# Performance work log

Measured on AMD Instinct MI355X. Metric: run time of the kernel, lower is better.

## Reference

```python
import jax, jax.numpy as jnp
import numpy as np

E = 256      # feat_dim
H = 4        # num_heads
D = E // H   # head_dim = 64
NC = 7       # num_classes
B = 65536
EPS = 1e-5


def layernorm(x, g, b):
    mu = jnp.mean(x, axis=-1, keepdims=True)
    var = jnp.mean((x - mu) ** 2, axis=-1, keepdims=True)
    return (x - mu) * jax.lax.rsqrt(var + EPS) * g + b


def setup_inputs() -> dict:
    key = jax.random.key(0)
    ks = jax.random.split(key, 16)
    s = 0.02
    return {
        "f_swin":   jax.random.normal(ks[0], (B, E), jnp.float32),
        "f_maxvit": jax.random.normal(ks[1], (B, E), jnp.float32),
        "f_focal":  jax.random.normal(ks[2], (B, E), jnp.float32),
        # MultiheadAttention params (torch packs q,k,v into in_proj)
        "in_proj_w": jax.random.normal(ks[3], (3 * E, E), jnp.float32) * s,
        "in_proj_b": jnp.zeros((3 * E,), jnp.float32),
        "out_w": jax.random.normal(ks[4], (E, E), jnp.float32) * s,
        "out_b": jnp.zeros((E,), jnp.float32),
        # fusion LayerNorm
        "ln1_g": jnp.ones((E,), jnp.float32),
        "ln1_b": jnp.zeros((E,), jnp.float32),
        # gate: Linear(3E, 3)
        "gate_w": jax.random.normal(ks[5], (3, 3 * E), jnp.float32) * s,
        "gate_b": jnp.zeros((3,), jnp.float32),
        # deep_head: LN -> Linear(E,256) -> GELU -> Linear(256,128) -> GELU -> Linear(128,7)
        "ln2_g": jnp.ones((E,), jnp.float32),
        "ln2_b": jnp.zeros((E,), jnp.float32),
        "w1": jax.random.normal(ks[6], (256, E), jnp.float32) * s,
        "b1": jnp.zeros((256,), jnp.float32),
        "w2": jax.random.normal(ks[7], (128, 256), jnp.float32) * s,
        "b2": jnp.zeros((128,), jnp.float32),
        "w3": jax.random.normal(ks[8], (NC, 128), jnp.float32) * s,
        "b3": jnp.zeros((NC,), jnp.float32),
    }


def reference(f_swin, f_maxvit, f_focal, in_proj_w, in_proj_b, out_w, out_b,
              ln1_g, ln1_b, gate_w, gate_b, ln2_g, ln2_b,
              w1, b1, w2, b2, w3, b3):
    # --- AttentionFusionModule ---
    stacked = jnp.stack([f_swin, f_maxvit, f_focal], axis=1)  # [B,3,E]
    qkv = stacked @ in_proj_w.T + in_proj_b                   # [B,3,3E]
    q, k, v = jnp.split(qkv, 3, axis=-1)
    # [B,3,E] -> [B,H,3,D]
    def to_heads(t):
        return t.reshape(t.shape[0], 3, H, D).transpose(0, 2, 1, 3)
    qh, kh, vh = to_heads(q), to_heads(k), to_heads(v)
    scores = jnp.einsum('bhqd,bhkd->bhqk', qh, kh) / jnp.sqrt(jnp.float32(D))
    attn = jax.nn.softmax(scores, axis=-1)
    ctx = jnp.einsum('bhqk,bhkd->bhqd', attn, vh)             # [B,H,3,D]
    ctx = ctx.transpose(0, 2, 1, 3).reshape(-1, 3, E)         # [B,3,E]
    att_out = ctx @ out_w.T + out_b
    x = layernorm(att_out + stacked, ln1_g, ln1_b)            # [B,3,E]
    concat = jnp.concatenate([f_swin, f_maxvit, f_focal], axis=-1)  # [B,3E]
    weights = jax.nn.softmax(concat @ gate_w.T + gate_b, axis=-1)   # [B,3]
    fused = jnp.einsum('bse,bs->be', x, weights)              # [B,E]
    # --- deep_head (Dropout inactive at inference; exact GELU as in torch) ---
    h = layernorm(fused, ln2_g, ln2_b)
    h = jax.nn.gelu(h @ w1.T + b1, approximate=False)
    h = jax.nn.gelu(h @ w2.T + b2, approximate=False)
    logits = h @ w3.T + b3
    return logits, fused
```

## Files before the change

kernel.cpp:

```cpp
#include <hip/hip_runtime.h>
#include <math.h>


#define E   256
#define NC  7
#define BM  16
#define TOK 48
#define NT  256
#define BS  264

typedef unsigned short u16;
typedef unsigned int   u32;
typedef __attribute__((ext_vector_type(8))) short  short8;
typedef __attribute__((ext_vector_type(4))) float  f32x4;

#define O_IPW 0
#define O_OW  196608
#define O_GW  262144
#define O_W1  264448
#define O_W2  329984
#define CVT_TOTAL 362752

__device__ __forceinline__ float bf2f(u32 u) { return __uint_as_float(u << 16); }
__device__ __forceinline__ u16 f2bf(float f) {
    u32 u = __float_as_uint(f);
    return (u16)((u + 0x7fffu + ((u >> 16) & 1u)) >> 16);
}

__global__ void cvt_weights(const float* __restrict__ ipw, const float* __restrict__ ow,
                            const float* __restrict__ gw,  const float* __restrict__ w1,
                            const float* __restrict__ w2,  u16* __restrict__ ws) {
    int i4 = (blockIdx.x * 256 + threadIdx.x) * 4;
    if (i4 >= CVT_TOTAL) return;
    const float* src; int off;
    if      (i4 < O_OW)  { src = ipw; off = i4; }
    else if (i4 < O_GW)  { src = ow;  off = i4 - O_OW; }
    else if (i4 < O_W1)  { src = gw;  off = i4 - O_GW; }
    else if (i4 < O_W2)  { src = w1;  off = i4 - O_W1; }
    else                 { src = w2;  off = i4 - O_W2; }
    float4 v = *(const float4*)(src + off);
    ushort4 o;
    o.x = f2bf(v.x); o.y = f2bf(v.y); o.z = f2bf(v.z); o.w = f2bf(v.w);
    *(ushort4*)(ws + i4) = o;
}

template<int MT, int NTW>
__device__ __forceinline__ void mfma_gemm(const u16* aLds, int aRow0,
                                          const u16* __restrict__ bW, int rowBase,
                                          int lane, f32x4 acc[MT][NTW]) {
    const int l16 = lane & 15, quad = lane >> 4;
    #pragma unroll
    for (int m = 0; m < MT; ++m)
        #pragma unroll
        for (int j = 0; j < NTW; ++j) acc[m][j] = (f32x4){0.f, 0.f, 0.f, 0.f};
    #pragma unroll 2
    for (int ks = 0; ks < 8; ++ks) {
        short8 a[MT];
        #pragma unroll
        for (int m = 0; m < MT; ++m)
            a[m] = *(const short8*)(aLds + (size_t)(aRow0 + m * 16 + l16) * BS + ks * 32 + quad * 8);
        #pragma unroll
        for (int j = 0; j < NTW; ++j) {
            short8 b = *(const short8*)(bW + (size_t)(rowBase + j * 16 + l16) * 256 + ks * 32 + quad * 8);
            #pragma unroll
            for (int m = 0; m < MT; ++m)
                acc[m][j] = __builtin_amdgcn_mfma_f32_16x16x32_bf16(a[m], b, acc[m][j], 0, 0, 0);
        }
    }
}

__global__ __launch_bounds__(NT, 2)
void dhc_mfma_kernel(
    const float* __restrict__ f0, const float* __restrict__ f1, const float* __restrict__ f2,
    const float* __restrict__ ipb, const float* __restrict__ ob,
    const float* __restrict__ ln1g, const float* __restrict__ ln1b,
    const float* __restrict__ gb,
    const float* __restrict__ ln2g, const float* __restrict__ ln2b,
    const float* __restrict__ b1, const float* __restrict__ b2,
    const float* __restrict__ w3, const float* __restrict__ b3,
    const u16* __restrict__ ws, float* __restrict__ d_out, int nrows)
{
    __shared__ __align__(16) u16 s_x[TOK * BS];
    __shared__ __align__(16) u16 s_buf[TOK * BS];
    __shared__ float s_attn[BM][4][9];
    __shared__ float s_gp[BM][9];
    __shared__ float s_wgt[BM][3];
    __shared__ float s_mu[TOK], s_rstd[TOK];
    __shared__ float s_mu2[BM], s_rstd2[BM];

    const int tid  = threadIdx.x;
    const int wid  = tid >> 6, lane = tid & 63;
    const int l16  = lane & 15, quad = lane >> 4;
    const long long row0 = (long long)blockIdx.x * BM;
    const size_t fused_base = (size_t)nrows * NC;

    const u16* ipw_b = ws + O_IPW;
    const u16* ow_b  = ws + O_OW;
    const u16* gw_b  = ws + O_GW;
    const u16* w1_b  = ws + O_W1;
    const u16* w2_b  = ws + O_W2;

    #pragma unroll
    for (int it = 0; it < 12; ++it) {
        int id = it * NT + tid;
        int t  = id >> 6;
        int c4 = (id & 63) * 4;
        int s  = t >> 4, r = t & 15;
        float4 v = {0.f, 0.f, 0.f, 0.f};
        if (row0 + r < nrows) {
            const float* src = (s == 0 ? f0 : (s == 1 ? f1 : f2));
            v = *(const float4*)(src + (size_t)(row0 + r) * E + c4);
        }
        ushort4 o;
        o.x = f2bf(v.x); o.y = f2bf(v.y); o.z = f2bf(v.z); o.w = f2bf(v.w);
        *(ushort4*)(s_x + t * BS + c4) = o;
    }
    __syncthreads();

    for (int p = 0; p < 2; ++p) {
        const int rowBase = (wid < 2) ? (128 * p + 64 * wid) : (256 + 128 * p + 64 * (wid - 2));
        f32x4 acc[3][4];
        mfma_gemm<3, 4>(s_x, 0, ipw_b, rowBase, lane, acc);
        #pragma unroll
        for (int j = 0; j < 4; ++j) {
            int n = wid * 64 + j * 16 + l16;
            float bias = ipb[rowBase + j * 16 + l16];
            #pragma unroll
            for (int m = 0; m < 3; ++m)
                #pragma unroll
                for (int rr = 0; rr < 4; ++rr) {
                    int tok = m * 16 + quad * 4 + rr;
                    s_buf[tok * BS + n] = f2bf(acc[m][j][rr] + bias);
                }
        }
        __syncthreads();
        if (tid < 96) {
            int r = tid / 6, rem = tid % 6;
            int hh = rem / 3, i = rem % 3;
            int h = 2 * p + hh;
            float d0 = 0.f, d1 = 0.f, d2 = 0.f;
            const u16* qrow = s_buf + (i * 16 + r) * BS + hh * 64;
            const u16* k0 = s_buf + (0 * 16 + r) * BS + 128 + hh * 64;
            const u16* k1 = s_buf + (1 * 16 + r) * BS + 128 + hh * 64;
            const u16* k2 = s_buf + (2 * 16 + r) * BS + 128 + hh * 64;
            for (int d8 = 0; d8 < 8; ++d8) {
                short8 qv = *(const short8*)(qrow + d8 * 8);
                short8 a0 = *(const short8*)(k0 + d8 * 8);
                short8 a1 = *(const short8*)(k1 + d8 * 8);
                short8 a2 = *(const short8*)(k2 + d8 * 8);
                #pragma unroll
                for (int e = 0; e < 8; ++e) {
                    float q = bf2f((u32)(u16)qv[e]);
                    d0 += q * bf2f((u32)(u16)a0[e]);
                    d1 += q * bf2f((u32)(u16)a1[e]);
                    d2 += q * bf2f((u32)(u16)a2[e]);
                }
            }
            d0 *= 0.125f; d1 *= 0.125f; d2 *= 0.125f;
            float mx = fmaxf(d0, fmaxf(d1, d2));
            float e0 = expf(d0 - mx), e1 = expf(d1 - mx), e2 = expf(d2 - mx);
            float inv = 1.f / (e0 + e1 + e2);
            s_attn[r][h][i * 3 + 0] = e0 * inv;
            s_attn[r][h][i * 3 + 1] = e1 * inv;
            s_attn[r][h][i * 3 + 2] = e2 * inv;
        }
        __syncthreads();
    }

    {
        const int rowBase = 512 + 64 * wid;
        f32x4 acc[3][4];
        mfma_gemm<3, 4>(s_x, 0, ipw_b, rowBase, lane, acc);
        #pragma unroll
        for (int j = 0; j < 4; ++j) {
            int n = wid * 64 + j * 16 + l16;
            float bias = ipb[rowBase + j * 16 + l16];
            #pragma unroll
            for (int m = 0; m < 3; ++m)
                #pragma unroll
                for (int rr = 0; rr < 4; ++rr) {
                    int tok = m * 16 + quad * 4 + rr;
                    s_buf[tok * BS + n] = f2bf(acc[m][j][rr] + bias);
                }
        }
    }
    __syncthreads();

    {
        int r = tid >> 4;
        int cb = (tid & 15) * 16;
        int h = cb >> 6;
        float a[9];
        #pragma unroll
        for (int q2 = 0; q2 < 9; ++q2) a[q2] = s_attn[r][h][q2];
        #pragma unroll
        for (int cc = 0; cc < 16; ++cc) {
            int c = cb + cc;
            float v0 = bf2f((u32)s_buf[(0 * 16 + r) * BS + c]);
            float v1 = bf2f((u32)s_buf[(1 * 16 + r) * BS + c]);
            float v2 = bf2f((u32)s_buf[(2 * 16 + r) * BS + c]);
            float c0 = a[0] * v0 + a[1] * v1 + a[2] * v2;
            float c1 = a[3] * v0 + a[4] * v1 + a[5] * v2;
            float c2 = a[6] * v0 + a[7] * v1 + a[8] * v2;
            s_buf[(0 * 16 + r) * BS + c] = f2bf(c0);
            s_buf[(1 * 16 + r) * BS + c] = f2bf(c1);
            s_buf[(2 * 16 + r) * BS + c] = f2bf(c2);
        }
    }
    __syncthreads();

    {
        const int rowBase = 64 * wid;
        f32x4 acc[3][4];
        mfma_gemm<3, 4>(s_buf, 0, ow_b, rowBase, lane, acc);
        #pragma unroll
        for (int j = 0; j < 4; ++j) {
            int n = rowBase + j * 16 + l16;
            float bias = ob[n];
            #pragma unroll
            for (int m = 0; m < 3; ++m)
                #pragma unroll
                for (int rr = 0; rr < 4; ++rr) {
                    int tok = m * 16 + quad * 4 + rr;
                    acc[m][j][rr] += bias + bf2f((u32)s_x[tok * BS + n]);
                }
        }
        __syncthreads();
        #pragma unroll
        for (int j = 0; j < 4; ++j) {
            int n = rowBase + j * 16 + l16;
            #pragma unroll
            for (int m = 0; m < 3; ++m)
                #pragma unroll
                for (int rr = 0; rr < 4; ++rr) {
                    int tok = m * 16 + quad * 4 + rr;
                    s_buf[tok * BS + n] = f2bf(acc[m][j][rr]);
                }
        }
    }
    __syncthreads();

    if (tid < TOK) {
        const u16* xp = s_buf + tid * BS;
        float sum = 0.f, sq = 0.f;
        for (int c8 = 0; c8 < 32; ++c8) {
            short8 v = *(const short8*)(xp + c8 * 8);
            #pragma unroll
            for (int e = 0; e < 8; ++e) {
                float x = bf2f((u32)(u16)v[e]);
                sum += x; sq += x * x;
            }
        }
        float mu = sum * (1.f / 256.f);
        float var = sq * (1.f / 256.f) - mu * mu;
        s_mu[tid] = mu;
        s_rstd[tid] = rsqrtf(var + 1e-5f);
    }
    __syncthreads();
    {
        float g = ln1g[tid], b = ln1b[tid];
        #pragma unroll 4
        for (int t = 0; t < TOK; ++t) {
            float x = bf2f((u32)s_buf[t * BS + tid]);
            s_buf[t * BS + tid] = f2bf((x - s_mu[t]) * s_rstd[t] * g + b);
        }
    }
    __syncthreads();

    if (tid < 144) {
        int r = tid / 9, rem = tid % 9;
        int g = rem / 3, s = rem % 3;
        const u16* xp = s_x + (s * 16 + r) * BS;
        const u16* wp = gw_b + g * 768 + s * 256;
        float acc = 0.f;
        for (int c8 = 0; c8 < 32; ++c8) {
            short8 xv = *(const short8*)(xp + c8 * 8);
            short8 wv = *(const short8*)(wp + c8 * 8);
            #pragma unroll
            for (int e = 0; e < 8; ++e)
                acc += bf2f((u32)(u16)xv[e]) * bf2f((u32)(u16)wv[e]);
        }
        s_gp[r][g * 3 + s] = acc;
    }
    __syncthreads();
    if (tid < 48) {
        int r = tid / 3, g = tid % 3;
        s_wgt[r][g] = gb[g] + s_gp[r][g * 3 + 0] + s_gp[r][g * 3 + 1] + s_gp[r][g * 3 + 2];
    }
    __syncthreads();
    if (tid < BM) {
        float l0 = s_wgt[tid][0], l1 = s_wgt[tid][1], l2 = s_wgt[tid][2];
        float mx = fmaxf(l0, fmaxf(l1, l2));
        float e0 = expf(l0 - mx), e1 = expf(l1 - mx), e2 = expf(l2 - mx);
        float inv = 1.f / (e0 + e1 + e2);
        s_wgt[tid][0] = e0 * inv; s_wgt[tid][1] = e1 * inv; s_wgt[tid][2] = e2 * inv;
    }
    __syncthreads();

    {
        int c = tid;
        float* outF = d_out + fused_base;
        #pragma unroll 4
        for (int r = 0; r < BM; ++r) {
            float f = s_wgt[r][0] * bf2f((u32)s_buf[(0 * 16 + r) * BS + c])
                    + s_wgt[r][1] * bf2f((u32)s_buf[(1 * 16 + r) * BS + c])
                    + s_wgt[r][2] * bf2f((u32)s_buf[(2 * 16 + r) * BS + c]);
            if (row0 + r < nrows) outF[(size_t)(row0 + r) * E + c] = f;
            s_buf[r * BS + c] = f2bf(f);
        }
    }
    __syncthreads();

    if (tid < BM) {
        const u16* fp = s_buf + tid * BS;
        float sum = 0.f, sq = 0.f;
        for (int c8 = 0; c8 < 32; ++c8) {
            short8 v = *(const short8*)(fp + c8 * 8);
            #pragma unroll
            for (int e = 0; e < 8; ++e) {
                float x = bf2f((u32)(u16)v[e]);
                sum += x; sq += x * x;
            }
        }
        float mu = sum * (1.f / 256.f);
        float var = sq * (1.f / 256.f) - mu * mu;
        s_mu2[tid] = mu;
        s_rstd2[tid] = rsqrtf(var + 1e-5f);
    }
    __syncthreads();
    {
        float g = ln2g[tid], b = ln2b[tid];
        #pragma unroll
        for (int r = 0; r < BM; ++r) {
            float x = bf2f((u32)s_buf[r * BS + tid]);
            s_buf[r * BS + tid] = f2bf((x - s_mu2[r]) * s_rstd2[r] * g + b);
        }
    }
    __syncthreads();

    {
        const int rowBase = 64 * wid;
        f32x4 acc[1][4];
        mfma_gemm<1, 4>(s_buf, 0, w1_b, rowBase, lane, acc);
        __syncthreads();
        #pragma unroll
        for (int j = 0; j < 4; ++j) {
            int n = rowBase + j * 16 + l16;
            float bias = b1[n];
            #pragma unroll
            for (int rr = 0; rr < 4; ++rr) {
                int r = quad * 4 + rr;
                float x = acc[0][j][rr] + bias;
                float hgelu = 0.5f * x * (1.f + erff(x * 0.70710678118654752f));
                s_buf[(16 + r) * BS + n] = f2bf(hgelu);
            }
        }
    }
    __syncthreads();

    {
        const int rowBase = 32 * wid;
        f32x4 acc[1][2];
        mfma_gemm<1, 2>(s_buf, 16, w2_b, rowBase, lane, acc);
        __syncthreads();
        #pragma unroll
        for (int j = 0; j < 2; ++j) {
            int n = rowBase + j * 16 + l16;
            float bias = b2[n];
            #pragma unroll
            for (int rr = 0; rr < 4; ++rr) {
                int r = quad * 4 + rr;
                float x = acc[0][j][rr] + bias;
                float hgelu = 0.5f * x * (1.f + erff(x * 0.70710678118654752f));
                s_buf[(32 + r) * BS + n] = f2bf(hgelu);
            }
        }
    }
    __syncthreads();

    if (tid < BM * NC) {
        int r = tid / NC, n = tid % NC;
        float acc = b3[n];
        const float* wr = w3 + n * 128;
        const u16* hp = s_buf + (32 + r) * BS;
        for (int k4 = 0; k4 < 32; ++k4) {
            float4 w = *(const float4*)(wr + k4 * 4);
            acc += bf2f((u32)hp[k4 * 4 + 0]) * w.x
                 + bf2f((u32)hp[k4 * 4 + 1]) * w.y
                 + bf2f((u32)hp[k4 * 4 + 2]) * w.z
                 + bf2f((u32)hp[k4 * 4 + 3]) * w.w;
        }
        if (row0 + r < nrows) d_out[(size_t)(row0 + r) * NC + n] = acc;
    }
}

extern "C" void kernel_launch(void* const* d_in, const int* in_sizes, int n_in,
                              void* d_out, int out_size, void* d_ws, size_t ws_size,
                              hipStream_t stream) {
    (void)n_in; (void)ws_size; (void)out_size;
    const int nrows = in_sizes[0] / E;
    u16* ws = (u16*)d_ws;
    cvt_weights<<<(CVT_TOTAL / 4 + 255) / 256, 256, 0, stream>>>(
        (const float*)d_in[3], (const float*)d_in[5], (const float*)d_in[9],
        (const float*)d_in[13], (const float*)d_in[15], ws);
    const int nblocks = (nrows + BM - 1) / BM;
    dhc_mfma_kernel<<<nblocks, NT, 0, stream>>>(
        (const float*)d_in[0], (const float*)d_in[1], (const float*)d_in[2],
        (const float*)d_in[4], (const float*)d_in[6],
        (const float*)d_in[7], (const float*)d_in[8],
        (const float*)d_in[10],
        (const float*)d_in[11], (const float*)d_in[12],
        (const float*)d_in[14], (const float*)d_in[16],
        (const float*)d_in[17], (const float*)d_in[18],
        ws, (float*)d_out, nrows);
}
```

Measured before the change: 708.5 us.

## Prefetch next GEMM weight tiles into registers while consuming current ones

Splits the MFMA GEMM into a weight-issue phase and a consume phase. Each stage's bf16 weight fragments are loaded into registers ahead of time, during the previous stage's epilogue and attention work, so global-load latency overlaps with compute instead of stalling inside the MFMA loop. This holds 32 short8 fragments (128 VGPRs) plus 16 more for the w2 stage, which risks spills or lower occupancy under launch_bounds(256,2).

```diff
diff --git a/kernel.cpp b/kernel.cpp
--- a/kernel.cpp
+++ b/kernel.cpp
@@ -44,28 +44,36 @@
     *(ushort4*)(ws + i4) = o;
 }
 
+template<int NTW>
+__device__ __forceinline__ void issue_b(const u16* __restrict__ bW, int rowBase, int lane,
+                                        short8 (&b)[8][NTW]) {
+    const int l16 = lane & 15, quad = lane >> 4;
+    #pragma unroll
+    for (int ks = 0; ks < 8; ++ks)
+        #pragma unroll
+        for (int j = 0; j < NTW; ++j)
+            b[ks][j] = *(const short8*)(bW + (size_t)(rowBase + j * 16 + l16) * 256 + ks * 32 + quad * 8);
+}
+
 template<int MT, int NTW>
-__device__ __forceinline__ void mfma_gemm(const u16* aLds, int aRow0,
-                                          const u16* __restrict__ bW, int rowBase,
-                                          int lane, f32x4 acc[MT][NTW]) {
+__device__ __forceinline__ void consume_gemm(const u16* aLds, int aRow0, int lane,
+                                             const short8 (&b)[8][NTW], f32x4 (&acc)[MT][NTW]) {
     const int l16 = lane & 15, quad = lane >> 4;
     #pragma unroll
     for (int m = 0; m < MT; ++m)
         #pragma unroll
         for (int j = 0; j < NTW; ++j) acc[m][j] = (f32x4){0.f, 0.f, 0.f, 0.f};
-    #pragma unroll 2
+    #pragma unroll
     for (int ks = 0; ks < 8; ++ks) {
         short8 a[MT];
         #pragma unroll
         for (int m = 0; m < MT; ++m)
             a[m] = *(const short8*)(aLds + (size_t)(aRow0 + m * 16 + l16) * BS + ks * 32 + quad * 8);
         #pragma unroll
-        for (int j = 0; j < NTW; ++j) {
-            short8 b = *(const short8*)(bW + (size_t)(rowBase + j * 16 + l16) * 256 + ks * 32 + quad * 8);
+        for (int j = 0; j < NTW; ++j)
             #pragma unroll
             for (int m = 0; m < MT; ++m)
-                acc[m][j] = __builtin_amdgcn_mfma_f32_16x16x32_bf16(a[m], b, acc[m][j], 0, 0, 0);
-        }
+                acc[m][j] = __builtin_amdgcn_mfma_f32_16x16x32_bf16(a[m], b[ks][j], acc[m][j], 0, 0, 0);
     }
 }
 
@@ -100,6 +108,13 @@
     const u16* w1_b  = ws + O_W1;
     const u16* w2_b  = ws + O_W2;
 
+    short8 bq[8][4];
+    short8 b5[8][2];
+
+    const int rb0 = (wid < 2) ? (64 * wid) : (256 + 64 * (wid - 2));
+
+    issue_b<4>(ipw_b, rb0, lane, bq);
+
     #pragma unroll
     for (int it = 0; it < 12; ++it) {
         int id = it * NT + tid;
@@ -118,13 +133,14 @@
     __syncthreads();
 
     for (int p = 0; p < 2; ++p) {
-        const int rowBase = (wid < 2) ? (128 * p + 64 * wid) : (256 + 128 * p + 64 * (wid - 2));
+        const int rb = rb0 + 128 * p;
         f32x4 acc[3][4];
-        mfma_gemm<3, 4>(s_x, 0, ipw_b, rowBase, lane, acc);
+        consume_gemm<3, 4>(s_x, 0, lane, bq, acc);
+        issue_b<4>(ipw_b, (p == 0) ? (rb0 + 128) : (512 + 64 * wid), lane, bq);
         #pragma unroll
         for (int j = 0; j < 4; ++j) {
             int n = wid * 64 + j * 16 + l16;
-            float bias = ipb[rowBase + j * 16 + l16];
+            float bias = ipb[rb + j * 16 + l16];
             #pragma unroll
             for (int m = 0; m < 3; ++m)
                 #pragma unroll
@@ -168,13 +184,14 @@
     }
 
     {
-        const int rowBase = 512 + 64 * wid;
+        const int rb = 512 + 64 * wid;
         f32x4 acc[3][4];
-        mfma_gemm<3, 4>(s_x, 0, ipw_b, rowBase, lane, acc);
+        consume_gemm<3, 4>(s_x, 0, lane, bq, acc);
+        issue_b<4>(ow_b, 64 * wid, lane, bq);
         #pragma unroll
         for (int j = 0; j < 4; ++j) {
             int n = wid * 64 + j * 16 + l16;
-            float bias = ipb[rowBase + j * 16 + l16];
+            float bias = ipb[rb + j * 16 + l16];
             #pragma unroll
             for (int m = 0; m < 3; ++m)
                 #pragma unroll
@@ -210,12 +227,13 @@
     __syncthreads();
 
     {
-        const int rowBase = 64 * wid;
+        const int rb = 64 * wid;
         f32x4 acc[3][4];
-        mfma_gemm<3, 4>(s_buf, 0, ow_b, rowBase, lane, acc);
+        consume_gemm<3, 4>(s_buf, 0, lane, bq, acc);
+        issue_b<4>(w1_b, 64 * wid, lane, bq);
         #pragma unroll
         for (int j = 0; j < 4; ++j) {
-            int n = rowBase + j * 16 + l16;
+            int n = rb + j * 16 + l16;
             float bias = ob[n];
             #pragma unroll
             for (int m = 0; m < 3; ++m)
@@ -228,7 +246,7 @@
         __syncthreads();
         #pragma unroll
         for (int j = 0; j < 4; ++j) {
-            int n = rowBase + j * 16 + l16;
+            int n = rb + j * 16 + l16;
             #pragma unroll
             for (int m = 0; m < 3; ++m)
                 #pragma unroll
@@ -339,13 +357,14 @@
     __syncthreads();
 
     {
-        const int rowBase = 64 * wid;
+        const int rb = 64 * wid;
         f32x4 acc[1][4];
-        mfma_gemm<1, 4>(s_buf, 0, w1_b, rowBase, lane, acc);
+        consume_gemm<1, 4>(s_buf, 0, lane, bq, acc);
+        issue_b<2>(w2_b, 32 * wid, lane, b5);
         __syncthreads();
         #pragma unroll
         for (int j = 0; j < 4; ++j) {
-            int n = rowBase + j * 16 + l16;
+            int n = rb + j * 16 + l16;
             float bias = b1[n];
             #pragma unroll
             for (int rr = 0; rr < 4; ++rr) {
@@ -359,13 +378,13 @@
     __syncthreads();
 
     {
-        const int rowBase = 32 * wid;
+        const int rb = 32 * wid;
         f32x4 acc[1][2];
-        mfma_gemm<1, 2>(s_buf, 16, w2_b, rowBase, lane, acc);
+        consume_gemm<1, 2>(s_buf, 16, lane, b5, acc);
         __syncthreads();
         #pragma unroll
         for (int j = 0; j < 2; ++j) {
-            int n = rowBase + j * 16 + l16;
+            int n = rb + j * 16 + l16;
             float bias = b2[n];
             #pragma unroll
             for (int rr = 0; rr < 4; ++rr) {
```

Result: no change. 720.1 us (+1.6%).
